# Kernel tuning notes

Hardware: AMD Instinct MI355X
Metric: run time of the kernel (lower is better)

The kernel has to match this reference:

```python
import jax, jax.numpy as jnp
import numpy as np

HEADS = 4
DIM_HEAD = 32
LN_EPS = 1e-5


def _ln_linear(x, g, b, W, bias):
    # LayerNorm over last dim then Linear (W stored as [in, out])
    mu = x.mean(-1, keepdims=True)
    var = ((x - mu) ** 2).mean(-1, keepdims=True)
    xn = (x - mu) * jax.lax.rsqrt(var + LN_EPS) * g + b
    return xn @ W + bias


def setup_inputs() -> dict:
    key = jax.random.key(0)
    ks = jax.random.split(key, 12)
    b, n, X, Y, W1, W2, d = 1, 6, 8, 8, 8, 8, 128
    x, y, w1, w2 = 8, 8, 8, 10
    inner = HEADS * DIM_HEAD  # 128
    s = 1.0 / np.sqrt(d)
    inp = {
        'q': jax.random.normal(ks[0], (b, n, X, Y, W1, W2, d), jnp.float32),
        'k': jax.random.normal(ks[1], (b, n, x, y, w1, w2, d), jnp.float32),
        'v': jax.random.normal(ks[2], (b, n, x, y, w1, w2, d), jnp.float32),
        'skip': jax.random.normal(ks[3], (b, X, Y, W1, W2, d), jnp.float32),
        'attn_scale': jnp.full((b,), 1.2, jnp.float32),
        'lnq_g': jnp.ones((d,), jnp.float32), 'lnq_b': jnp.zeros((d,), jnp.float32),
        'Wq': jax.random.normal(ks[4], (d, inner), jnp.float32) * s,
        'bq': jnp.zeros((inner,), jnp.float32),
        'lnk_g': jnp.ones((d,), jnp.float32), 'lnk_b': jnp.zeros((d,), jnp.float32),
        'Wk': jax.random.normal(ks[5], (d, inner), jnp.float32) * s,
        'bk': jnp.zeros((inner,), jnp.float32),
        'lnv_g': jnp.ones((d,), jnp.float32), 'lnv_b': jnp.zeros((d,), jnp.float32),
        'Wv': jax.random.normal(ks[6], (d, inner), jnp.float32) * s,
        'bv': jnp.zeros((inner,), jnp.float32),
        'Wp': jax.random.normal(ks[7], (inner, d), jnp.float32) * s,
        'bp': jnp.zeros((d,), jnp.float32),
    }
    return inp


def reference(q, k, v, skip, attn_scale, lnq_g, lnq_b, Wq, bq, lnk_g, lnk_b, Wk, bk,
              lnv_g, lnv_b, Wv, bv, Wp, bp):
    b, n, X, Y, W1, W2, d = q.shape
    _, _, x, y, w1, w2, _ = k.shape
    m, dh = HEADS, DIM_HEAD
    scale = dh ** -0.5
    # 'b n x y w1 w2 d -> b (x y) (n w1 w2) d'
    qf = jnp.transpose(q, (0, 2, 3, 1, 4, 5, 6)).reshape(b, X * Y, n * W1 * W2, d)
    kf = jnp.transpose(k, (0, 2, 3, 1, 4, 5, 6)).reshape(b, x * y, n * w1 * w2, d)
    vf = jnp.transpose(v, (0, 2, 3, 1, 4, 5, 6)).reshape(b, x * y, n * w1 * w2, d)
    qp = _ln_linear(qf, lnq_g, lnq_b, Wq, bq)
    kp = _ln_linear(kf, lnk_g, lnk_b, Wk, bk)
    vp = _ln_linear(vf, lnv_g, lnv_b, Wv, bv)

    def split_heads(t):  # 'b L N (m d) -> (b m) L N d'
        B, L, N, _ = t.shape
        return jnp.transpose(t.reshape(B, L, N, m, dh), (0, 3, 1, 2, 4)).reshape(B * m, L, N, dh)

    qh, kh, vh = split_heads(qp), split_heads(kp), split_heads(vp)
    dot = scale * jnp.einsum('blqd,blkd->blqk', qh, kh)  # (b*m, L, Q, K)
    # per-batch scale factor repeated over heads (b-major, matching einops '(b m)')
    sv = jnp.repeat(attn_scale.reshape(-1), m)
    dot = dot * sv[:, None, None, None]
    att = jax.nn.softmax(dot, axis=-1)
    a = jnp.einsum('blqk,blkd->blqd', att, vh)
    # '(b m) L N d -> b L N (m d)'
    a = jnp.transpose(a.reshape(b, m, X * Y, n * W1 * W2, dh), (0, 2, 3, 1, 4))
    a = a.reshape(b, X * Y, n * W1 * W2, m * dh)
    # 'b (x y) (n w1 w2) d -> b n x y w1 w2 d'
    a = a.reshape(b, X, Y, n, W1, W2, m * dh)
    a = jnp.transpose(a, (0, 3, 1, 2, 4, 5, 6))
    z = a @ Wp + bp        # proj
    z = z.mean(axis=1)     # mean over views n
    return z + skip
```

## Files before the change

kernel.cpp:

```cpp
#include <hip/hip_runtime.h>

#define D 128
#define LN_EPS 1e-5f
#define PSTRD 20
#define WSTR 136

typedef __attribute__((ext_vector_type(8))) short short8;
typedef __attribute__((ext_vector_type(4))) float f32x4;

static __device__ __forceinline__ unsigned short f2bf(float f) {
    union { float f; unsigned u; } v; v.f = f;
    unsigned r = v.u + 0x7fffu + ((v.u >> 16) & 1u);
    return (unsigned short)(r >> 16);
}
static __device__ __forceinline__ unsigned pack2(float a, float b) {
    return (unsigned)f2bf(a) | ((unsigned)f2bf(b) << 16);
}
static __device__ __forceinline__ float bf2f(unsigned short u) {
    union { unsigned u; float f; } v; v.u = ((unsigned)u) << 16; return v.f;
}

__global__ __launch_bounds__(64)
void wprep_kernel(const float* __restrict__ Wq, const float* __restrict__ Wk,
                  const float* __restrict__ Wv, const float* __restrict__ Wp,
                  const float* __restrict__ gq, const float* __restrict__ betaq,
                  const float* __restrict__ biasq,
                  const float* __restrict__ gk, const float* __restrict__ betak,
                  const float* __restrict__ biask,
                  const float* __restrict__ gv, const float* __restrict__ betav,
                  const float* __restrict__ biasv,
                  unsigned* __restrict__ Wt, unsigned* __restrict__ Wpt,
                  float* __restrict__ c1, float* __restrict__ c2)
{
    const int id = blockIdx.x;
    const int w  = id >> 7;
    const int o  = id & 127;
    const int t  = threadIdx.x;
    if (w < 3) {
        const float* W  = (w == 0) ? Wq : (w == 1) ? Wk : Wv;
        const float* gg = (w == 0) ? gq : (w == 1) ? gk : gv;
        const float* bb = (w == 0) ? betaq : (w == 1) ? betak : betav;
        const float* bi = (w == 0) ? biasq : (w == 1) ? biask : biasv;
        const float w0 = W[(2 * t) * 128 + o];
        const float w1 = W[(2 * t + 1) * 128 + o];
        const float g0 = gg[2 * t], g1 = gg[2 * t + 1];
        const float b0 = bb[2 * t], b1 = bb[2 * t + 1];
        Wt[((size_t)w * 128 + o) * 64 + t] = pack2(g0 * w0, g1 * w1);
        float s1 = g0 * w0 + g1 * w1;
        float s2 = b0 * w0 + b1 * w1;
        #pragma unroll
        for (int off = 32; off > 0; off >>= 1) {
            s1 += __shfl_down(s1, off, 64);
            s2 += __shfl_down(s2, off, 64);
        }
        if (t == 0) { c1[w * 128 + o] = s1; c2[w * 128 + o] = s2 + bi[o]; }
    } else {
        Wpt[(size_t)o * 64 + t] = pack2(Wp[(2 * t) * 128 + o], Wp[(2 * t + 1) * 128 + o]);
    }
}

template<int PERL, int W1W2, int W2D, int MODE>
static __device__ __forceinline__
void ln_body(const float* __restrict__ in,
             const unsigned short* __restrict__ wlds,
             const float* __restrict__ c1, const float* __restrict__ c2,
             unsigned short* __restrict__ out,
             float scale, int rowbase, int t,
             float (*smu)[16], float (*ssq)[16])
{
    const int wv   = t >> 6;
    const int lane = t & 63;
    const int m16  = lane & 15;
    const int g    = lane >> 4;
    const int row  = rowbase + wv * 16 + m16;

    const int l   = row / PERL, j = row - l * PERL;
    const int n   = j / W1W2, rem = j - n * W1W2;
    const int w1  = rem / W2D, w2 = rem - w1 * W2D;
    const int X   = l >> 3, Y = l & 7;
    const float* xrow = in + ((size_t)(((n * 8 + X) * 8 + Y) * 8 + w1) * W2D + w2) * D;

    short8 xf[4];
    #pragma unroll
    for (int kt = 0; kt < 4; ++kt) {
        const float4 a = *(const float4*)(xrow + kt * 32 + g * 8);
        const float4 b = *(const float4*)(xrow + kt * 32 + g * 8 + 4);
        short8 vv;
        vv[0] = (short)f2bf(a.x); vv[1] = (short)f2bf(a.y);
        vv[2] = (short)f2bf(a.z); vv[3] = (short)f2bf(a.w);
        vv[4] = (short)f2bf(b.x); vv[5] = (short)f2bf(b.y);
        vv[6] = (short)f2bf(b.z); vv[7] = (short)f2bf(b.w);
        xf[kt] = vv;
    }

    short8 ones;
    #pragma unroll
    for (int jj = 0; jj < 8; ++jj) ones[jj] = (short)0x3F80;
    f32x4 sums = {0.f, 0.f, 0.f, 0.f}, gram = {0.f, 0.f, 0.f, 0.f};
    #pragma unroll
    for (int kt = 0; kt < 4; ++kt) {
        sums = __builtin_amdgcn_mfma_f32_16x16x32_bf16(xf[kt], ones, sums, 0, 0, 0);
        gram = __builtin_amdgcn_mfma_f32_16x16x32_bf16(xf[kt], xf[kt], gram, 0, 0, 0);
    }
    if (g == (m16 >> 2)) {
        smu[wv][m16] = sums[m16 & 3];
        ssq[wv][m16] = gram[m16 & 3];
    }
    __syncthreads();
    const float mu   = smu[wv][m16] * (1.0f / 128.0f);
    const float msq  = ssq[wv][m16] * (1.0f / 128.0f);
    const float rstd = rsqrtf(msq - mu * mu + LN_EPS);
    const float rmu  = rstd * mu;

    f32x4 acc[8] = {{0,0,0,0},{0,0,0,0},{0,0,0,0},{0,0,0,0},
                    {0,0,0,0},{0,0,0,0},{0,0,0,0},{0,0,0,0}};
    #pragma unroll
    for (int kt = 0; kt < 4; ++kt) {
        #pragma unroll
        for (int ot = 0; ot < 8; ++ot) {
            const short8 aw = *(const short8*)&wlds[
                (ot * 16 + m16) * WSTR + kt * 32 + g * 8];
            acc[ot] = __builtin_amdgcn_mfma_f32_16x16x32_bf16(aw, xf[kt], acc[ot], 0, 0, 0);
        }
    }

    #pragma unroll
    for (int ot = 0; ot < 8; ++ot) {
        const int ob = ot * 16 + g * 4;
        const float4 cc1 = *(const float4*)&c1[ob];
        const float4 cc2 = *(const float4*)&c2[ob];
        float v0 = rstd * acc[ot][0] - rmu * cc1.x + cc2.x;
        float v1 = rstd * acc[ot][1] - rmu * cc1.y + cc2.y;
        float v2 = rstd * acc[ot][2] - rmu * cc1.z + cc2.z;
        float v3 = rstd * acc[ot][3] - rmu * cc1.w + cc2.w;
        if (MODE == 1) { v0 *= scale; v1 *= scale; v2 *= scale; v3 *= scale; }
        if (MODE == 2) {
            const float vals[4] = {v0, v1, v2, v3};
            #pragma unroll
            for (int c = 0; c < 4; ++c) {
                const int d = ob + c;
                out[((size_t)((l * 4 + (d >> 5)) * 32 + (d & 31))) * 480 + j] = f2bf(vals[c]);
            }
        } else {
            *(ushort4*)&out[(size_t)row * D + ob] =
                make_ushort4(f2bf(v0), f2bf(v1), f2bf(v2), f2bf(v3));
        }
    }
}

__global__ __launch_bounds__(256, 4)
void ln_fused_kernel(const float* __restrict__ q, const float* __restrict__ k,
                     const float* __restrict__ v,
                     const unsigned short* __restrict__ Wt,
                     const float* __restrict__ c1, const float* __restrict__ c2,
                     unsigned short* __restrict__ qbuf,
                     unsigned short* __restrict__ kbuf,
                     unsigned short* __restrict__ vtb,
                     const float* __restrict__ scale_p)
{
    __shared__ __align__(16) unsigned short wlds[128 * WSTR];
    __shared__ float smu[4][16];
    __shared__ float ssq[4][16];

    const int bid = blockIdx.x;
    const int t   = threadIdx.x;

    const unsigned short* Wsrc =
        (bid < 384) ? Wt : (bid < 864) ? (Wt + 16384) : (Wt + 32768);

    {
        const uint4* ws = (const uint4*)Wsrc;
        #pragma unroll
        for (int i = 0; i < 8; ++i) {
            const int idx = i * 256 + t;
            const int r = idx >> 4, s = idx & 15;
            *(uint4*)&wlds[r * WSTR + s * 8] = ws[idx];
        }
    }
    __syncthreads();

    if (bid < 384) {
        const float s = scale_p[0] * 0.17677669529663687f * 1.4426950408889634f;
        ln_body<384, 64, 8, 1>(q, wlds, c1, c2, qbuf, s, bid * 64, t, smu, ssq);
    } else if (bid < 864) {
        ln_body<480, 80, 10, 0>(k, wlds, c1 + 128, c2 + 128, kbuf,
                                1.0f, (bid - 384) * 64, t, smu, ssq);
    } else {
        ln_body<480, 80, 10, 2>(v, wlds, c1 + 256, c2 + 256, vtb,
                                1.0f, (bid - 864) * 64, t, smu, ssq);
    }
}

__global__ __launch_bounds__(384)
void attn_kernel(const unsigned short* __restrict__ qb,
                 const unsigned short* __restrict__ kb,
                 const unsigned short* __restrict__ vtb,
                 unsigned short* __restrict__ out)
{
    __shared__ __align__(16) unsigned Pall[6 * 16 * PSTRD];

    const int l    = blockIdx.x;
    const int h    = blockIdx.y;
    const int qz   = blockIdx.z;
    const int t    = threadIdx.x;
    const int wv   = t >> 6;
    const int lane = t & 63;
    const int m16  = lane & 15;
    const int g    = lane >> 4;

    unsigned* P = &Pall[wv * 16 * PSTRD];
    const unsigned short* PS = (const unsigned short*)P;

    const int qrow0 = qz * 96 + wv * 16;
    const short8 bq = *(const short8*)(
        qb + ((size_t)(l * 384 + qrow0 + m16)) * 128 + h * 32 + g * 8);

    const unsigned short* kbase = kb + ((size_t)l * 480) * 128 + h * 32;
    const unsigned short* vbase = vtb + ((size_t)(l * 4 + h) * 32) * 480;

    f32x4 o0 = {0.f, 0.f, 0.f, 0.f};
    f32x4 o1 = {0.f, 0.f, 0.f, 0.f};
    float esum = 0.f;

    #pragma unroll 3
    for (int kc = 0; kc < 15; ++kc) {
        const short8 a0 = *(const short8*)(kbase + (size_t)(kc * 32 + m16) * 128 + g * 8);
        const short8 a1 = *(const short8*)(kbase + (size_t)(kc * 32 + 16 + m16) * 128 + g * 8);
        const f32x4 z = {0.f, 0.f, 0.f, 0.f};
        const f32x4 s0 = __builtin_amdgcn_mfma_f32_16x16x32_bf16(a0, bq, z, 0, 0, 0);
        const f32x4 s1 = __builtin_amdgcn_mfma_f32_16x16x32_bf16(a1, bq, z, 0, 0, 0);

        float e0[4], e1[4];
        #pragma unroll
        for (int r = 0; r < 4; ++r) {
            e0[r] = __builtin_amdgcn_exp2f(s0[r]);
            e1[r] = __builtin_amdgcn_exp2f(s1[r]);
            esum += e0[r] + e1[r];
        }

        uint2 pk0, pk1;
        pk0.x = pack2(e0[0], e0[1]); pk0.y = pack2(e0[2], e0[3]);
        pk1.x = pack2(e1[0], e1[1]); pk1.y = pack2(e1[2], e1[3]);
        *(uint2*)&P[m16 * PSTRD + 2 * g]     = pk0;
        *(uint2*)&P[m16 * PSTRD + 8 + 2 * g] = pk1;

        const short8 bp  = *(const short8*)&PS[m16 * 40 + g * 8];
        const short8 av0 = *(const short8*)(vbase + (size_t)m16 * 480 + kc * 32 + g * 8);
        const short8 av1 = *(const short8*)(vbase + (size_t)(16 + m16) * 480 + kc * 32 + g * 8);
        o0 = __builtin_amdgcn_mfma_f32_16x16x32_bf16(av0, bp, o0, 0, 0, 0);
        o1 = __builtin_amdgcn_mfma_f32_16x16x32_bf16(av1, bp, o1, 0, 0, 0);
    }

    float lsum = esum;
    lsum += __shfl_xor(lsum, 16, 64);
    lsum += __shfl_xor(lsum, 32, 64);
    const float linv = 1.0f / lsum;

    unsigned short* ob = out + ((size_t)(l * 384 + qrow0 + m16)) * 128 + h * 32;
    *(ushort4*)(ob + g * 4) = make_ushort4(
        f2bf(o0[0] * linv), f2bf(o0[1] * linv), f2bf(o0[2] * linv), f2bf(o0[3] * linv));
    *(ushort4*)(ob + 16 + g * 4) = make_ushort4(
        f2bf(o1[0] * linv), f2bf(o1[1] * linv), f2bf(o1[2] * linv), f2bf(o1[3] * linv));
}

__global__ __launch_bounds__(256)
void proj_kernel(const unsigned short* __restrict__ attnb,
                 const unsigned short* __restrict__ Wpt,
                 const float* __restrict__ bp,
                 const float* __restrict__ skip,
                 float* __restrict__ out)
{
    const int t    = threadIdx.x;
    const int wv   = t >> 6;
    const int lane = t & 63;
    const int m16  = lane & 15;
    const int g    = lane >> 4;

    const int row  = blockIdx.x * 16 + m16;
    const int l    = row >> 6;
    const int qrem = row & 63;

    short8 xf[4];
    #pragma unroll
    for (int kt = 0; kt < 4; ++kt) {
        float m[8] = {0,0,0,0,0,0,0,0};
        #pragma unroll
        for (int n = 0; n < 6; ++n) {
            const short8 vv = *(const short8*)(
                attnb + ((size_t)(l * 384 + n * 64 + qrem)) * 128 + kt * 32 + g * 8);
            #pragma unroll
            for (int jj = 0; jj < 8; ++jj)
                m[jj] += bf2f((unsigned short)vv[jj]);
        }
        short8 pk;
        #pragma unroll
        for (int jj = 0; jj < 8; ++jj) pk[jj] = (short)f2bf(m[jj] * (1.0f / 6.0f));
        xf[kt] = pk;
    }

    f32x4 acc[2] = {{0,0,0,0},{0,0,0,0}};
    #pragma unroll
    for (int kt = 0; kt < 4; ++kt) {
        #pragma unroll
        for (int ot = 0; ot < 2; ++ot) {
            const short8 aw = *(const short8*)&Wpt[
                (size_t)((wv * 2 + ot) * 16 + m16) * 128 + kt * 32 + g * 8];
            acc[ot] = __builtin_amdgcn_mfma_f32_16x16x32_bf16(aw, xf[kt], acc[ot], 0, 0, 0);
        }
    }

    #pragma unroll
    for (int ot = 0; ot < 2; ++ot) {
        const int ob = (wv * 2 + ot) * 16 + g * 4;
        const float4 bb = *(const float4*)&bp[ob];
        const float4 sk = *(const float4*)&skip[(size_t)row * D + ob];
        float4 r;
        r.x = acc[ot][0] + bb.x + sk.x;
        r.y = acc[ot][1] + bb.y + sk.y;
        r.z = acc[ot][2] + bb.z + sk.z;
        r.w = acc[ot][3] + bb.w + sk.w;
        *(float4*)&out[(size_t)row * D + ob] = r;
    }
}

extern "C" void kernel_launch(void* const* d_in, const int* in_sizes, int n_in,
                              void* d_out, int out_size, void* d_ws, size_t ws_size,
                              hipStream_t stream)
{
    const float* q          = (const float*)d_in[0];
    const float* k          = (const float*)d_in[1];
    const float* v          = (const float*)d_in[2];
    const float* skip       = (const float*)d_in[3];
    const float* attn_scale = (const float*)d_in[4];
    const float* lnq_g      = (const float*)d_in[5];
    const float* lnq_b      = (const float*)d_in[6];
    const float* Wq         = (const float*)d_in[7];
    const float* bq         = (const float*)d_in[8];
    const float* lnk_g      = (const float*)d_in[9];
    const float* lnk_b      = (const float*)d_in[10];
    const float* Wk         = (const float*)d_in[11];
    const float* bk         = (const float*)d_in[12];
    const float* lnv_g      = (const float*)d_in[13];
    const float* lnv_b      = (const float*)d_in[14];
    const float* Wv         = (const float*)d_in[15];
    const float* bv         = (const float*)d_in[16];
    const float* Wp         = (const float*)d_in[17];
    const float* bp         = (const float*)d_in[18];

    float* out = (float*)d_out;
    char*  wsb = (char*)d_ws;

    unsigned short* qbuf  = (unsigned short*)(wsb);
    unsigned short* kbuf  = (unsigned short*)(wsb + 6291456);
    unsigned short* vtb   = (unsigned short*)(wsb + 14155776);
    unsigned short* Wt    = (unsigned short*)(wsb + 22020096);
    unsigned short* Wpt   = (unsigned short*)(wsb + 22118400);
    float*          c1    = (float*)        (wsb + 22151168);
    float*          c2    = (float*)        (wsb + 22152704);
    unsigned short* attnb = (unsigned short*)(wsb + 22154240);

    wprep_kernel<<<512, 64, 0, stream>>>(Wq, Wk, Wv, Wp,
                                         lnq_g, lnq_b, bq,
                                         lnk_g, lnk_b, bk,
                                         lnv_g, lnv_b, bv,
                                         (unsigned*)Wt, (unsigned*)Wpt, c1, c2);

    ln_fused_kernel<<<1344, 256, 0, stream>>>(q, k, v, Wt, c1, c2,
                                              qbuf, kbuf, vtb, attn_scale);

    dim3 agrid(64, 4, 4);
    attn_kernel<<<agrid, 384, 0, stream>>>(qbuf, kbuf, vtb, attnb);

    proj_kernel<<<256, 256, 0, stream>>>(attnb, Wpt, bp, skip, out);
}
```

Baseline: 166.4 us.

## Replace LDS round-trips with shuffles and software-prefetch K/V in attention

The LayerNorm kernel now gets row statistics from the MFMA outputs through wave shuffles instead of shared memory plus a block barrier. Each block processes two 64-row chunks, which halves the grid and amortises the weight load into LDS. The attention kernel rebuilds the P operand with cross-lane shuffles instead of writing and re-reading LDS, and prefetches the next K/V chunk into registers. It also moves from 6 to 4 waves per block over a larger grid. The costs are more shuffle and select instructions, higher register pressure from the prefetched operands, and fewer blocks in the LN kernel.

```diff
diff --git a/kernel.cpp b/kernel.cpp
--- a/kernel.cpp
+++ b/kernel.cpp
@@ -2,7 +2,6 @@
 
 #define D 128
 #define LN_EPS 1e-5f
-#define PSTRD 20
 #define WSTR 136
 
 typedef __attribute__((ext_vector_type(8))) short short8;
@@ -65,8 +64,7 @@
              const unsigned short* __restrict__ wlds,
              const float* __restrict__ c1, const float* __restrict__ c2,
              unsigned short* __restrict__ out,
-             float scale, int rowbase, int t,
-             float (*smu)[16], float (*ssq)[16])
+             float scale, int rowbase, int t)
 {
     const int wv   = t >> 6;
     const int lane = t & 63;
@@ -102,13 +100,17 @@
         sums = __builtin_amdgcn_mfma_f32_16x16x32_bf16(xf[kt], ones, sums, 0, 0, 0);
         gram = __builtin_amdgcn_mfma_f32_16x16x32_bf16(xf[kt], xf[kt], gram, 0, 0, 0);
     }
-    if (g == (m16 >> 2)) {
-        smu[wv][m16] = sums[m16 & 3];
-        ssq[wv][m16] = gram[m16 & 3];
-    }
-    __syncthreads();
-    const float mu   = smu[wv][m16] * (1.0f / 128.0f);
-    const float msq  = ssq[wv][m16] * (1.0f / 128.0f);
+    const int su = ((m16 >> 2) << 4) | m16;
+    const float s0 = __shfl(sums[0], su, 64), s1 = __shfl(sums[1], su, 64);
+    const float s2 = __shfl(sums[2], su, 64), s3 = __shfl(sums[3], su, 64);
+    const float q0 = __shfl(gram[0], su, 64), q1 = __shfl(gram[1], su, 64);
+    const float q2 = __shfl(gram[2], su, 64), q3 = __shfl(gram[3], su, 64);
+    const int rr = m16 & 3;
+    const float rs = (rr == 0) ? s0 : (rr == 1) ? s1 : (rr == 2) ? s2 : s3;
+    const float rq = (rr == 0) ? q0 : (rr == 1) ? q1 : (rr == 2) ? q2 : q3;
+
+    const float mu   = rs * (1.0f / 128.0f);
+    const float msq  = rq * (1.0f / 128.0f);
     const float rstd = rsqrtf(msq - mu * mu + LN_EPS);
     const float rmu  = rstd * mu;
 
@@ -159,14 +161,12 @@
                      const float* __restrict__ scale_p)
 {
     __shared__ __align__(16) unsigned short wlds[128 * WSTR];
-    __shared__ float smu[4][16];
-    __shared__ float ssq[4][16];
 
     const int bid = blockIdx.x;
     const int t   = threadIdx.x;
 
     const unsigned short* Wsrc =
-        (bid < 384) ? Wt : (bid < 864) ? (Wt + 16384) : (Wt + 32768);
+        (bid < 192) ? Wt : (bid < 432) ? (Wt + 16384) : (Wt + 32768);
 
     {
         const uint4* ws = (const uint4*)Wsrc;
@@ -179,26 +179,28 @@
     }
     __syncthreads();
 
-    if (bid < 384) {
+    if (bid < 192) {
         const float s = scale_p[0] * 0.17677669529663687f * 1.4426950408889634f;
-        ln_body<384, 64, 8, 1>(q, wlds, c1, c2, qbuf, s, bid * 64, t, smu, ssq);
-    } else if (bid < 864) {
-        ln_body<480, 80, 10, 0>(k, wlds, c1 + 128, c2 + 128, kbuf,
-                                1.0f, (bid - 384) * 64, t, smu, ssq);
+        const int rb = bid * 128;
+        ln_body<384, 64, 8, 1>(q, wlds, c1, c2, qbuf, s, rb, t);
+        ln_body<384, 64, 8, 1>(q, wlds, c1, c2, qbuf, s, rb + 64, t);
+    } else if (bid < 432) {
+        const int rb = (bid - 192) * 128;
+        ln_body<480, 80, 10, 0>(k, wlds, c1 + 128, c2 + 128, kbuf, 1.0f, rb, t);
+        ln_body<480, 80, 10, 0>(k, wlds, c1 + 128, c2 + 128, kbuf, 1.0f, rb + 64, t);
     } else {
-        ln_body<480, 80, 10, 2>(v, wlds, c1 + 256, c2 + 256, vtb,
-                                1.0f, (bid - 864) * 64, t, smu, ssq);
-    }
-}
-
-__global__ __launch_bounds__(384)
+        const int rb = (bid - 432) * 128;
+        ln_body<480, 80, 10, 2>(v, wlds, c1 + 256, c2 + 256, vtb, 1.0f, rb, t);
+        ln_body<480, 80, 10, 2>(v, wlds, c1 + 256, c2 + 256, vtb, 1.0f, rb + 64, t);
+    }
+}
+
+__global__ __launch_bounds__(256, 4)
 void attn_kernel(const unsigned short* __restrict__ qb,
                  const unsigned short* __restrict__ kb,
                  const unsigned short* __restrict__ vtb,
                  unsigned short* __restrict__ out)
 {
-    __shared__ __align__(16) unsigned Pall[6 * 16 * PSTRD];
-
     const int l    = blockIdx.x;
     const int h    = blockIdx.y;
     const int qz   = blockIdx.z;
@@ -208,10 +210,7 @@
     const int m16  = lane & 15;
     const int g    = lane >> 4;
 
-    unsigned* P = &Pall[wv * 16 * PSTRD];
-    const unsigned short* PS = (const unsigned short*)P;
-
-    const int qrow0 = qz * 96 + wv * 16;
+    const int qrow0 = qz * 64 + wv * 16;
     const short8 bq = *(const short8*)(
         qb + ((size_t)(l * 384 + qrow0 + m16)) * 128 + h * 32 + g * 8);
 
@@ -222,10 +221,25 @@
     f32x4 o1 = {0.f, 0.f, 0.f, 0.f};
     float esum = 0.f;
 
-    #pragma unroll 3
+    const int srcA = m16 + (g & 1) * 32;
+    const int srcB = srcA + 16;
+    const bool lo  = (g < 2);
+
+    short8 a0n = *(const short8*)(kbase + (size_t)(m16) * 128 + g * 8);
+    short8 a1n = *(const short8*)(kbase + (size_t)(16 + m16) * 128 + g * 8);
+    short8 v0n = *(const short8*)(vbase + (size_t)m16 * 480 + g * 8);
+    short8 v1n = *(const short8*)(vbase + (size_t)(16 + m16) * 480 + g * 8);
+
     for (int kc = 0; kc < 15; ++kc) {
-        const short8 a0 = *(const short8*)(kbase + (size_t)(kc * 32 + m16) * 128 + g * 8);
-        const short8 a1 = *(const short8*)(kbase + (size_t)(kc * 32 + 16 + m16) * 128 + g * 8);
+        const short8 a0 = a0n, a1 = a1n, v0 = v0n, v1 = v1n;
+        if (kc < 14) {
+            const int kn = (kc + 1) * 32;
+            a0n = *(const short8*)(kbase + (size_t)(kn + m16) * 128 + g * 8);
+            a1n = *(const short8*)(kbase + (size_t)(kn + 16 + m16) * 128 + g * 8);
+            v0n = *(const short8*)(vbase + (size_t)m16 * 480 + kn + g * 8);
+            v1n = *(const short8*)(vbase + (size_t)(16 + m16) * 480 + kn + g * 8);
+        }
+
         const f32x4 z = {0.f, 0.f, 0.f, 0.f};
         const f32x4 s0 = __builtin_amdgcn_mfma_f32_16x16x32_bf16(a0, bq, z, 0, 0, 0);
         const f32x4 s1 = __builtin_amdgcn_mfma_f32_16x16x32_bf16(a1, bq, z, 0, 0, 0);
@@ -238,17 +252,28 @@
             esum += e0[r] + e1[r];
         }
 
-        uint2 pk0, pk1;
-        pk0.x = pack2(e0[0], e0[1]); pk0.y = pack2(e0[2], e0[3]);
-        pk1.x = pack2(e1[0], e1[1]); pk1.y = pack2(e1[2], e1[3]);
-        *(uint2*)&P[m16 * PSTRD + 2 * g]     = pk0;
-        *(uint2*)&P[m16 * PSTRD + 8 + 2 * g] = pk1;
-
-        const short8 bp  = *(const short8*)&PS[m16 * 40 + g * 8];
-        const short8 av0 = *(const short8*)(vbase + (size_t)m16 * 480 + kc * 32 + g * 8);
-        const short8 av1 = *(const short8*)(vbase + (size_t)(16 + m16) * 480 + kc * 32 + g * 8);
-        o0 = __builtin_amdgcn_mfma_f32_16x16x32_bf16(av0, bp, o0, 0, 0, 0);
-        o1 = __builtin_amdgcn_mfma_f32_16x16x32_bf16(av1, bp, o1, 0, 0, 0);
+        const unsigned pA0 = pack2(e0[0], e0[1]);
+        const unsigned pA1 = pack2(e0[2], e0[3]);
+        const unsigned pB0 = pack2(e1[0], e1[1]);
+        const unsigned pB1 = pack2(e1[2], e1[3]);
+
+        const unsigned uA0 = __shfl(pA0, srcA, 64);
+        const unsigned uA1 = __shfl(pA1, srcA, 64);
+        const unsigned uA2 = __shfl(pA0, srcB, 64);
+        const unsigned uA3 = __shfl(pA1, srcB, 64);
+        const unsigned uB0 = __shfl(pB0, srcA, 64);
+        const unsigned uB1 = __shfl(pB1, srcA, 64);
+        const unsigned uB2 = __shfl(pB0, srcB, 64);
+        const unsigned uB3 = __shfl(pB1, srcB, 64);
+
+        union { unsigned u[4]; short8 s; } bp;
+        bp.u[0] = lo ? uA0 : uB0;
+        bp.u[1] = lo ? uA1 : uB1;
+        bp.u[2] = lo ? uA2 : uB2;
+        bp.u[3] = lo ? uA3 : uB3;
+
+        o0 = __builtin_amdgcn_mfma_f32_16x16x32_bf16(v0, bp.s, o0, 0, 0, 0);
+        o1 = __builtin_amdgcn_mfma_f32_16x16x32_bf16(v1, bp.s, o1, 0, 0, 0);
     }
 
     float lsum = esum;
@@ -365,11 +390,11 @@
                                          lnv_g, lnv_b, bv,
                                          (unsigned*)Wt, (unsigned*)Wpt, c1, c2);
 
-    ln_fused_kernel<<<1344, 256, 0, stream>>>(q, k, v, Wt, c1, c2,
-                                              qbuf, kbuf, vtb, attn_scale);
-
-    dim3 agrid(64, 4, 4);
-    attn_kernel<<<agrid, 384, 0, stream>>>(qbuf, kbuf, vtb, attnb);
+    ln_fused_kernel<<<672, 256, 0, stream>>>(q, k, v, Wt, c1, c2,
+                                             qbuf, kbuf, vtb, attn_scale);
+
+    dim3 agrid(64, 4, 6);
+    attn_kernel<<<agrid, 256, 0, stream>>>(qbuf, kbuf, vtb, attnb);
 
     proj_kernel<<<256, 256, 0, stream>>>(attnb, Wpt, bp, skip, out);
 }
```

Result: slower. 208.0 us (+25.0%).
